# Performance work log

Hardware: AMD Instinct MI355X
Metric: run time of the kernel (lower is better)

## Reference

```python
import jax, jax.numpy as jnp
import numpy as np

B, T, IN_DIM = 32, 1024, 32
E, H, P = 256, 4, 32  # embed_dim, heads, max_patches
HD = E // H


def _lin(x, w, b):
    # torch nn.Linear: y = x @ W.T + b, W: [out, in]
    return jnp.einsum('...i,oi->...o', x, w) + b


def setup_inputs() -> dict:
    key = jax.random.key(0)
    ks = jax.random.split(key, 13)
    s = 0.02
    return {
        'x': jax.random.normal(ks[0], (B, T, IN_DIM), jnp.float32),
        'ip_w': jax.random.normal(ks[1], (E, IN_DIM), jnp.float32) * s,
        'ip_b': jnp.zeros((E,), jnp.float32),
        'in_proj_w': jax.random.normal(ks[2], (3 * E, E), jnp.float32) * s,
        'in_proj_b': jnp.zeros((3 * E,), jnp.float32),
        'out_w': jax.random.normal(ks[3], (E, E), jnp.float32) * s,
        'out_b': jnp.zeros((E,), jnp.float32),
        'bp_w1': jax.random.normal(ks[4], (32, E), jnp.float32) * s,
        'bp_b1': jnp.zeros((32,), jnp.float32),
        'bp_w2': jax.random.normal(ks[5], (1, 32), jnp.float32) * s,
        'bp_b2': jnp.zeros((1,), jnp.float32),
        'pr_w': jax.random.normal(ks[6], (E, E), jnp.float32) * s,
        'pr_b': jnp.zeros((E,), jnp.float32),
    }


def reference(x, ip_w, ip_b, in_proj_w, in_proj_b, out_w, out_b,
              bp_w1, bp_b1, bp_w2, bp_b2, pr_w, pr_b):
    # input projection
    h = _lin(x, ip_w, ip_b)  # [B,T,E]
    # MultiheadAttention (self-attn, batch_first, eval/no-dropout)
    qkv = _lin(h, in_proj_w, in_proj_b)  # [B,T,3E]
    q, k, v = jnp.split(qkv, 3, axis=-1)
    q = q.reshape(B, T, H, HD)
    k = k.reshape(B, T, H, HD)
    v = v.reshape(B, T, H, HD)
    scores = jnp.einsum('bqhd,bkhd->bhqk', q, k) / jnp.sqrt(jnp.float32(HD))
    attn = jax.nn.softmax(scores, axis=-1)
    ctx = jnp.einsum('bhqk,bkhd->bqhd', attn, v).reshape(B, T, E)
    attn_out = _lin(ctx, out_w, out_b)  # [B,T,E]
    # boundary scores
    bscore = jax.nn.sigmoid(_lin(jax.nn.relu(_lin(attn_out, bp_w1, bp_b1)), bp_w2, bp_b2))[..., 0]  # [B,T]
    cbp = jnp.cumsum(bscore, axis=1)
    cbp = cbp / (cbp[:, -1:] + 1e-6)
    pid = jnp.minimum(jnp.floor(cbp * P).astype(jnp.int32), P - 1)  # [B,T]
    # segment-mean pooling via scatter-add
    b_idx = jnp.broadcast_to(jnp.arange(B)[:, None], (B, T))
    pe = jnp.zeros((B, P, E), attn_out.dtype).at[b_idx, pid].add(attn_out)
    cnt = jnp.zeros((B, P), attn_out.dtype).at[b_idx, pid].add(1.0)
    pe = pe / jnp.clip(cnt, 1.0)[..., None]
    return _lin(pe, pr_w, pr_b)  # [B,P,E]
```

## Files before the change

### kernel.cpp

```cpp
#include <hip/hip_runtime.h>
#include <math.h>

constexpr int Bn  = 32;
constexpr int Tn  = 1024;
constexpr int INn = 32;
constexpr int En  = 256;
constexpr int Pn  = 32;

typedef short bf16x8 __attribute__((ext_vector_type(8)));
typedef float f32x4  __attribute__((ext_vector_type(4)));

__device__ __forceinline__ unsigned short f2bf(float f) {
    unsigned int b = __float_as_uint(f);
    b += 0x7FFF + ((b >> 16) & 1);
    return (unsigned short)(b >> 16);
}
__device__ __forceinline__ float bf2f(unsigned short h) {
    return __uint_as_float(((unsigned int)h) << 16);
}

__global__ __launch_bounds__(256) void k_prep(const float* __restrict__ ipw,
                                              const float* __restrict__ ipb,
                                              const float* __restrict__ inw,
                                              const float* __restrict__ inb,
                                              const float* __restrict__ outw,
                                              const float* __restrict__ w1,
                                              unsigned short* __restrict__ Wcb,
                                              float* __restrict__ bc,
                                              unsigned short* __restrict__ Wb,
                                              unsigned short* __restrict__ w1h,
                                              unsigned short* __restrict__ w1l) {
    int blk = blockIdx.x, tid = threadIdx.x;
    if (blk < 96) {
        int idx = blk * 256 + tid;
        int o = idx >> 5, i = idx & 31;
        const float* wr = inw + (size_t)o * En;
        float a0 = 0.f, a1 = 0.f;
        for (int e = 0; e < En; e += 2) {
            a0 += wr[e]     * ipw[(size_t)e * INn + i];
            a1 += wr[e + 1] * ipw[(size_t)(e + 1) * INn + i];
        }
        Wcb[(size_t)o * INn + i] = f2bf(a0 + a1);
    } else if (blk < 99) {
        int o = (blk - 96) * 256 + tid;
        const float* wr = inw + (size_t)o * En;
        float a = inb[o];
        for (int e = 0; e < En; ++e) a += wr[e] * ipb[e];
        bc[o] = a;
    } else if (blk < 163) {
        int idx = (blk - 99) * 256 + tid;
        float4 a = *(const float4*)(outw + (size_t)idx * 4);
        unsigned int u0 = f2bf(a.x) | ((unsigned int)f2bf(a.y) << 16);
        unsigned int u1 = f2bf(a.z) | ((unsigned int)f2bf(a.w) << 16);
        *(uint2*)(Wb + (size_t)idx * 4) = make_uint2(u0, u1);
    } else {
        int idx = (blk - 163) * 256 + tid;
        float a = w1[idx];
        unsigned short h = f2bf(a);
        w1h[idx] = h;
        w1l[idx] = f2bf(a - bf2f(h));
    }
}

__global__ __launch_bounds__(256, 2) void k_qkv(const float* __restrict__ x,
                                                const unsigned short* __restrict__ Wcb,
                                                const float* __restrict__ bc,
                                                unsigned short* __restrict__ Qb,
                                                unsigned short* __restrict__ Kb,
                                                unsigned short* __restrict__ Vt) {
    int tid = threadIdx.x;
    int wv = tid >> 6, lane = tid & 63;
    int cl = lane & 15, quad = lane >> 4;
    int m0 = blockIdx.x * 64;
    int b = m0 >> 10, tl0 = m0 & 1023;
    int n0w = wv * 192;
    f32x4 zero4 = {0.f, 0.f, 0.f, 0.f};

    bf16x8 wfrag[12]; float bv[12];
#pragma unroll
    for (int nt = 0; nt < 12; ++nt) {
        int col = n0w + nt * 16 + cl;
        wfrag[nt] = *(const bf16x8*)(Wcb + (size_t)col * 32 + quad * 8);
        bv[nt] = bc[col];
    }
#pragma unroll
    for (int mt = 0; mt < 4; ++mt) {
        const float* xr = x + (size_t)(m0 + mt * 16 + cl) * 32 + quad * 8;
        float4 xa = *(const float4*)xr, xc = *(const float4*)(xr + 4);
        bf16x8 af;
        af[0] = (short)f2bf(xa.x); af[1] = (short)f2bf(xa.y);
        af[2] = (short)f2bf(xa.z); af[3] = (short)f2bf(xa.w);
        af[4] = (short)f2bf(xc.x); af[5] = (short)f2bf(xc.y);
        af[6] = (short)f2bf(xc.z); af[7] = (short)f2bf(xc.w);
        f32x4 acc[12];
#pragma unroll
        for (int nt = 0; nt < 12; ++nt)
            acc[nt] = __builtin_amdgcn_mfma_f32_16x16x32_bf16(af, wfrag[nt], zero4, 0, 0, 0);
        int tloc = tl0 + mt * 16 + quad * 4;
#pragma unroll
        for (int nt = 0; nt < 12; ++nt) {
            int col = n0w + nt * 16 + cl;
            int slot = col >> 8, c = col & 255;
            int h = c >> 6, d = c & 63;
            int bh = b * 4 + h;
            if (slot == 2) {
                unsigned int u0 = f2bf(acc[nt][0] + bv[nt]) |
                                  ((unsigned int)f2bf(acc[nt][1] + bv[nt]) << 16);
                unsigned int u1 = f2bf(acc[nt][2] + bv[nt]) |
                                  ((unsigned int)f2bf(acc[nt][3] + bv[nt]) << 16);
                *(uint2*)(Vt + ((size_t)bh * 64 + d) * 1024 + tloc) = make_uint2(u0, u1);
            } else {
                unsigned short* dst = (slot ? Kb : Qb) +
                                      ((size_t)bh * 1024 + tloc) * 64 + d;
#pragma unroll
                for (int r = 0; r < 4; ++r)
                    dst[(size_t)r * 64] = f2bf(acc[nt][r] + bv[nt]);
            }
        }
    }
}

__global__ __launch_bounds__(256, 4) void k_attn(const unsigned short* __restrict__ Qb,
                                                 const unsigned short* __restrict__ Kb,
                                                 const unsigned short* __restrict__ Vt,
                                                 unsigned short* __restrict__ Po0,
                                                 unsigned short* __restrict__ Po1,
                                                 float* __restrict__ L0,
                                                 float* __restrict__ L1) {
    __shared__ unsigned short Ks[64][72];
    __shared__ unsigned short Vs[64][72];
    __shared__ __align__(16) unsigned short Pl[4][2][16][40];
    int blk = blockIdx.x;
    int bh = blk & 127;
    int r_ = blk >> 7;
    int qb = r_ & 7, half = r_ >> 3;
    int b = bh >> 2, h = bh & 3;
    int tid = threadIdx.x;
    int wv = tid >> 6, lane = tid & 63;
    int cl = lane & 15, quad = lane >> 4;
    int qbase = qb * 128 + wv * 32;

    f32x4 zero4 = {0.f, 0.f, 0.f, 0.f};
    bf16x8 qfrag[2][2];
#pragma unroll
    for (int tt = 0; tt < 2; ++tt)
#pragma unroll
        for (int ch = 0; ch < 2; ++ch)
            qfrag[tt][ch] = *(const bf16x8*)(Qb +
                ((size_t)bh * 1024 + qbase + tt * 16 + cl) * 64 + ch * 32 + quad * 8);
    f32x4 acc[2][4];
#pragma unroll
    for (int tt = 0; tt < 2; ++tt)
#pragma unroll
        for (int dt = 0; dt < 4; ++dt) acc[tt][dt] = zero4;
    float l[2] = {0.f, 0.f};

    const unsigned short* Kbase = Kb + (size_t)bh * 65536;
    const unsigned short* Vbase = Vt + (size_t)bh * 65536;

    for (int kt = 0; kt < 8; ++kt) {
        int ktt = half * 8 + kt;
#pragma unroll
        for (int r = 0; r < 2; ++r) {
            int idx = r * 256 + tid; int row = idx >> 3, c16 = idx & 7;
            *(uint4*)&Ks[row][c16 * 8] =
                *(const uint4*)(Kbase + (size_t)(ktt * 64 + row) * 64 + c16 * 8);
            *(uint4*)&Vs[row][c16 * 8] =
                *(const uint4*)(Vbase + (size_t)row * 1024 + ktt * 64 + c16 * 8);
        }
        __syncthreads();
#pragma unroll
        for (int c = 0; c < 2; ++c) {
            bf16x8 ka0 = *(const bf16x8*)&Ks[c * 32 + cl][quad * 8];
            bf16x8 ka1 = *(const bf16x8*)&Ks[c * 32 + cl][32 + quad * 8];
            bf16x8 kb0 = *(const bf16x8*)&Ks[c * 32 + 16 + cl][quad * 8];
            bf16x8 kb1 = *(const bf16x8*)&Ks[c * 32 + 16 + cl][32 + quad * 8];
            bf16x8 va[4];
#pragma unroll
            for (int dt = 0; dt < 4; ++dt)
                va[dt] = *(const bf16x8*)&Vs[dt * 16 + cl][c * 32 + quad * 8];
#pragma unroll
            for (int tt = 0; tt < 2; ++tt) {
                f32x4 s0 = __builtin_amdgcn_mfma_f32_16x16x32_bf16(ka0, qfrag[tt][0], zero4, 0, 0, 0);
                s0 = __builtin_amdgcn_mfma_f32_16x16x32_bf16(ka1, qfrag[tt][1], s0, 0, 0, 0);
                f32x4 s1 = __builtin_amdgcn_mfma_f32_16x16x32_bf16(kb0, qfrag[tt][0], zero4, 0, 0, 0);
                s1 = __builtin_amdgcn_mfma_f32_16x16x32_bf16(kb1, qfrag[tt][1], s1, 0, 0, 0);
                float p0 = __expf(0.125f * s0[0]), p1 = __expf(0.125f * s0[1]);
                float p2 = __expf(0.125f * s0[2]), p3 = __expf(0.125f * s0[3]);
                float p4 = __expf(0.125f * s1[0]), p5 = __expf(0.125f * s1[1]);
                float p6 = __expf(0.125f * s1[2]), p7 = __expf(0.125f * s1[3]);
                l[tt] += ((p0 + p1) + (p2 + p3)) + ((p4 + p5) + (p6 + p7));
                unsigned int w0 = f2bf(p0) | ((unsigned int)f2bf(p1) << 16);
                unsigned int w1 = f2bf(p2) | ((unsigned int)f2bf(p3) << 16);
                unsigned int w2 = f2bf(p4) | ((unsigned int)f2bf(p5) << 16);
                unsigned int w3 = f2bf(p6) | ((unsigned int)f2bf(p7) << 16);
                *(uint2*)&Pl[wv][tt][cl][quad * 4]      = make_uint2(w0, w1);
                *(uint2*)&Pl[wv][tt][cl][16 + quad * 4] = make_uint2(w2, w3);
            }
            asm volatile("s_waitcnt lgkmcnt(0)" ::: "memory");
#pragma unroll
            for (int tt = 0; tt < 2; ++tt) {
                bf16x8 pf = *(const bf16x8*)&Pl[wv][tt][cl][quad * 8];
#pragma unroll
                for (int dt = 0; dt < 4; ++dt)
                    acc[tt][dt] = __builtin_amdgcn_mfma_f32_16x16x32_bf16(pf, va[dt], acc[tt][dt], 0, 0, 0);
            }
        }
        __syncthreads();
    }
#pragma unroll
    for (int tt = 0; tt < 2; ++tt) {
        l[tt] += __shfl_xor(l[tt], 16);
        l[tt] += __shfl_xor(l[tt], 32);
    }
    unsigned short* Po = half ? Po1 : Po0;
    float* Lp = half ? L1 : L0;
#pragma unroll
    for (int tt = 0; tt < 2; ++tt) {
#pragma unroll
        for (int r = 0; r < 4; ++r) {
            size_t row = (size_t)(b * 1024 + qbase + tt * 16 + quad * 4 + r) * En;
#pragma unroll
            for (int dt = 0; dt < 4; ++dt)
                Po[row + h * 64 + dt * 16 + cl] = f2bf(acc[tt][dt][r]);
        }
    }
    if (quad == 0) {
#pragma unroll
        for (int tt = 0; tt < 2; ++tt)
            Lp[bh * 1024 + qbase + tt * 16 + cl] = l[tt];
    }
}

__global__ __launch_bounds__(256) void k_out(const unsigned short* __restrict__ Po0,
                                             const unsigned short* __restrict__ Po1,
                                             const float* __restrict__ L0,
                                             const float* __restrict__ L1,
                                             const unsigned short* __restrict__ Wb,
                                             const float* __restrict__ bias,
                                             float* __restrict__ AO) {
    __shared__ unsigned short As[64][32];
    __shared__ unsigned short Bs[256][32];
    int tid = threadIdx.x;
    int wv = tid >> 6, lane = tid & 63;
    int cl = lane & 15, quad = lane >> 4;
    size_t m0 = (size_t)blockIdx.x * 64;

    f32x4 acc[4][4];
#pragma unroll
    for (int mt = 0; mt < 4; ++mt)
#pragma unroll
        for (int nt = 0; nt < 4; ++nt) acc[mt][nt] = {0.f, 0.f, 0.f, 0.f};

    for (int kt = 0; kt < 8; ++kt) {
        if (kt) __syncthreads();
        {
            int row = tid >> 2, c4 = tid & 3;
            size_t g = (m0 + row) * En + kt * 32 + c4 * 8;
            uint4 u0 = *(const uint4*)(Po0 + g);
            uint4 u1 = *(const uint4*)(Po1 + g);
            int gt = (int)(m0 + row);
            int li = ((gt >> 10) * 4 + (kt >> 1)) * 1024 + (gt & 1023);
            float linv = 1.f / (L0[li] + L1[li]);
            unsigned int a0[4] = {u0.x, u0.y, u0.z, u0.w};
            unsigned int a1[4] = {u1.x, u1.y, u1.z, u1.w};
            unsigned int w[4];
#pragma unroll
            for (int j = 0; j < 4; ++j) {
                float lo = (bf2f((unsigned short)(a0[j] & 0xffff)) +
                            bf2f((unsigned short)(a1[j] & 0xffff))) * linv;
                float hi = (bf2f((unsigned short)(a0[j] >> 16)) +
                            bf2f((unsigned short)(a1[j] >> 16))) * linv;
                w[j] = f2bf(lo) | ((unsigned int)f2bf(hi) << 16);
            }
            *(uint4*)&As[row][c4 * 8] = make_uint4(w[0], w[1], w[2], w[3]);
        }
#pragma unroll
        for (int j = 0; j < 4; ++j) {
            int lin = j * 256 + tid; int n = lin >> 2, c = lin & 3;
            *(uint4*)&Bs[n][c * 8] =
                *(const uint4*)(Wb + (size_t)n * En + kt * 32 + c * 8);
        }
        __syncthreads();
        bf16x8 af[4], bfr[4];
#pragma unroll
        for (int mt = 0; mt < 4; ++mt)
            af[mt] = *(const bf16x8*)&As[mt * 16 + cl][quad * 8];
#pragma unroll
        for (int nt = 0; nt < 4; ++nt)
            bfr[nt] = *(const bf16x8*)&Bs[wv * 64 + nt * 16 + cl][quad * 8];
#pragma unroll
        for (int mt = 0; mt < 4; ++mt)
#pragma unroll
            for (int nt = 0; nt < 4; ++nt)
                acc[mt][nt] = __builtin_amdgcn_mfma_f32_16x16x32_bf16(af[mt], bfr[nt], acc[mt][nt], 0, 0, 0);
    }
    float bv[4];
#pragma unroll
    for (int nt = 0; nt < 4; ++nt) bv[nt] = bias[wv * 64 + nt * 16 + cl];
#pragma unroll
    for (int mt = 0; mt < 4; ++mt)
#pragma unroll
        for (int nt = 0; nt < 4; ++nt)
#pragma unroll
            for (int r = 0; r < 4; ++r)
                AO[(m0 + mt * 16 + quad * 4 + r) * En + wv * 64 + nt * 16 + cl] =
                    acc[mt][nt][r] + bv[nt];
}

__global__ __launch_bounds__(256) void k_bscore(const float* __restrict__ AO,
                                                const unsigned short* __restrict__ w1h,
                                                const unsigned short* __restrict__ w1l,
                                                const float* __restrict__ b1,
                                                const float* __restrict__ w2,
                                                const float* __restrict__ b2,
                                                float* __restrict__ bsc) {
    __shared__ unsigned short Ah[128][72];
    __shared__ unsigned short Al[128][72];
    int tid = threadIdx.x;
    int wv = tid >> 6, lane = tid & 63;
    int cl = lane & 15, quad = lane >> 4;
    int m0 = blockIdx.x * 128;

    f32x4 acc[2][2];
#pragma unroll
    for (int mt = 0; mt < 2; ++mt)
#pragma unroll
        for (int nt = 0; nt < 2; ++nt) acc[mt][nt] = {0.f, 0.f, 0.f, 0.f};

    for (int kt = 0; kt < 4; ++kt) {
        if (kt) __syncthreads();
#pragma unroll
        for (int j = 0; j < 8; ++j) {
            int lin = j * 256 + tid; int row = lin >> 4, c4 = lin & 15;
            float4 a = *(const float4*)(AO + (size_t)(m0 + row) * En + kt * 64 + c4 * 4);
            unsigned short h0 = f2bf(a.x), h1v = f2bf(a.y), h2 = f2bf(a.z), h3 = f2bf(a.w);
            unsigned short l0 = f2bf(a.x - bf2f(h0)), l1v = f2bf(a.y - bf2f(h1v));
            unsigned short l2 = f2bf(a.z - bf2f(h2)), l3 = f2bf(a.w - bf2f(h3));
            *(uint2*)&Ah[row][c4 * 4] =
                make_uint2(h0 | ((unsigned int)h1v << 16), h2 | ((unsigned int)h3 << 16));
            *(uint2*)&Al[row][c4 * 4] =
                make_uint2(l0 | ((unsigned int)l1v << 16), l2 | ((unsigned int)l3 << 16));
        }
        __syncthreads();
#pragma unroll
        for (int ks = 0; ks < 2; ++ks) {
            bf16x8 bh_[2], bl_[2];
#pragma unroll
            for (int nt = 0; nt < 2; ++nt) {
                size_t off = (size_t)(nt * 16 + cl) * En + kt * 64 + ks * 32 + quad * 8;
                bh_[nt] = *(const bf16x8*)(w1h + off);
                bl_[nt] = *(const bf16x8*)(w1l + off);
            }
#pragma unroll
            for (int mt = 0; mt < 2; ++mt) {
                int row = wv * 32 + mt * 16 + cl;
                bf16x8 ah = *(const bf16x8*)&Ah[row][ks * 32 + quad * 8];
                bf16x8 al = *(const bf16x8*)&Al[row][ks * 32 + quad * 8];
#pragma unroll
                for (int nt = 0; nt < 2; ++nt) {
                    acc[mt][nt] = __builtin_amdgcn_mfma_f32_16x16x32_bf16(ah, bh_[nt], acc[mt][nt], 0, 0, 0);
                    acc[mt][nt] = __builtin_amdgcn_mfma_f32_16x16x32_bf16(ah, bl_[nt], acc[mt][nt], 0, 0, 0);
                    acc[mt][nt] = __builtin_amdgcn_mfma_f32_16x16x32_bf16(al, bh_[nt], acc[mt][nt], 0, 0, 0);
                }
            }
        }
    }
    float b1v[2], w2v[2];
#pragma unroll
    for (int nt = 0; nt < 2; ++nt) {
        b1v[nt] = b1[nt * 16 + cl];
        w2v[nt] = w2[nt * 16 + cl];
    }
    float b2v = b2[0];
#pragma unroll
    for (int mt = 0; mt < 2; ++mt) {
        f32x4 z;
#pragma unroll
        for (int r = 0; r < 4; ++r)
            z[r] = fmaxf(acc[mt][0][r] + b1v[0], 0.f) * w2v[0] +
                   fmaxf(acc[mt][1][r] + b1v[1], 0.f) * w2v[1];
#pragma unroll
        for (int d = 1; d < 16; d <<= 1)
#pragma unroll
            for (int r = 0; r < 4; ++r) z[r] += __shfl_xor(z[r], d);
        if (cl == 0) {
#pragma unroll
            for (int r = 0; r < 4; ++r)
                bsc[m0 + wv * 32 + mt * 16 + quad * 4 + r] =
                    1.f / (1.f + __expf(-(z[r] + b2v)));
        }
    }
}

__global__ __launch_bounds__(1024) void k_scan(const float* __restrict__ bsc,
                                               int* __restrict__ segs) {
    __shared__ float wsum[16];
    __shared__ float s_pre[1024];
    __shared__ float s_tot;
    int b = blockIdx.x, t = threadIdx.x;
    float x = bsc[b * Tn + t];
#pragma unroll
    for (int d = 1; d < 64; d <<= 1) {
        float y = __shfl_up(x, d);
        if ((t & 63) >= d) x += y;
    }
    int w = t >> 6;
    if ((t & 63) == 63) wsum[w] = x;
    __syncthreads();
    if (t == 0) {
        float s = 0.f;
        for (int i = 0; i < 16; ++i) { float tmp = wsum[i]; wsum[i] = s; s += tmp; }
        s_tot = s;
    }
    __syncthreads();
    float pre = x + wsum[w];
    s_pre[t] = pre;
    __syncthreads();
    float denom = s_tot + 1e-6f;
    float qv = pre / denom * 32.0f;
    int pid = min((int)floorf(qv), 31);
    int pidprev = -1;
    if (t > 0) {
        float qp = s_pre[t - 1] / denom * 32.0f;
        pidprev = min((int)floorf(qp), 31);
    }
    for (int p = pidprev + 1; p <= pid; ++p) segs[b * 33 + p] = t;
    if (t == 1023)
        for (int p = pid + 1; p <= 32; ++p) segs[b * 33 + p] = Tn;
}

__global__ __launch_bounds__(256) void k_pool_proj(const float* __restrict__ ao,
                                                   const int* __restrict__ segs,
                                                   const float* __restrict__ prw,
                                                   const float* __restrict__ prb,
                                                   float* __restrict__ out) {
    __shared__ float pes[En];
    int b = blockIdx.y, p = blockIdx.x;
    int s = segs[b * 33 + p];
    int e = segs[b * 33 + p + 1];
    int tid = threadIdx.x;
    float sum = 0.f;
    for (int t = s; t < e; ++t)
        sum += ao[((size_t)b * Tn + t) * En + tid];
    pes[tid] = sum / fmaxf((float)(e - s), 1.f);
    __syncthreads();
    float a0 = prb[tid], a1 = 0.f;
#pragma unroll
    for (int k = 0; k < En; k += 4) {
        float4 wv = *(const float4*)(prw + (size_t)tid * En + k);
        float4 pv = *(const float4*)&pes[k];
        a0 += wv.x * pv.x; a1 += wv.y * pv.y;
        a0 += wv.z * pv.z; a1 += wv.w * pv.w;
    }
    out[((size_t)b * Pn + p) * En + tid] = a0 + a1;
}

extern "C" void kernel_launch(void* const* d_in, const int* in_sizes, int n_in,
                              void* d_out, int out_size, void* d_ws, size_t ws_size,
                              hipStream_t stream) {
    const float* x    = (const float*)d_in[0];
    const float* ipw  = (const float*)d_in[1];
    const float* ipb  = (const float*)d_in[2];
    const float* inw  = (const float*)d_in[3];
    const float* inb  = (const float*)d_in[4];
    const float* outw = (const float*)d_in[5];
    const float* outb = (const float*)d_in[6];
    const float* bw1  = (const float*)d_in[7];
    const float* bb1  = (const float*)d_in[8];
    const float* bw2  = (const float*)d_in[9];
    const float* bb2  = (const float*)d_in[10];
    const float* prw  = (const float*)d_in[11];
    const float* prb  = (const float*)d_in[12];

    char* base = (char*)d_ws;
    unsigned short* Qb  = (unsigned short*)base;
    unsigned short* Kb  = Qb + (size_t)8388608;
    float*          AO  = (float*)base;
    unsigned short* Vt  = (unsigned short*)(base + (size_t)33554432);
    unsigned short* Po0 = (unsigned short*)(base + (size_t)50331648);
    unsigned short* Po1 = (unsigned short*)(base + (size_t)67108864);
    unsigned short* Wcb = (unsigned short*)(base + (size_t)83886080);
    float*          bc  = (float*)(base + (size_t)83935232);
    unsigned short* Wb  = (unsigned short*)(base + (size_t)83938304);
    unsigned short* w1h = (unsigned short*)(base + (size_t)84069376);
    unsigned short* w1l = (unsigned short*)(base + (size_t)84085760);
    float*          L0  = (float*)(base + (size_t)84102144);
    float*          L1  = (float*)(base + (size_t)84626432);
    float*          bsc = (float*)(base + (size_t)85150720);
    int*           segs = (int*)(base + (size_t)85281792);

    k_prep<<<195, 256, 0, stream>>>(ipw, ipb, inw, inb, outw, bw1,
                                    Wcb, bc, Wb, w1h, w1l);
    k_qkv<<<512, 256, 0, stream>>>(x, Wcb, bc, Qb, Kb, Vt);
    k_attn<<<2048, 256, 0, stream>>>(Qb, Kb, Vt, Po0, Po1, L0, L1);
    k_out<<<512, 256, 0, stream>>>(Po0, Po1, L0, L1, Wb, outb, AO);
    k_bscore<<<256, 256, 0, stream>>>(AO, w1h, w1l, bb1, bw2, bb2, bsc);
    k_scan<<<32, 1024, 0, stream>>>(bsc, segs);
    k_pool_proj<<<dim3(32, 32), 256, 0, stream>>>(AO, segs, prw, prb,
                                                  (float*)d_out);
}
```

Before: 237.8 us.

## Split pool/projection into MFMA split-bf16 GEMM and use truncating perm pack in attention

The fused pool+projection kernel, where each thread did a scalar 256-length dot product per patch, is split into a pooling kernel that writes patch means to workspace and a final kernel. The final kernel runs the 1024x256x256 projection with bf16 MFMA, using hi/lo weight and activation splits (three products) to keep accuracy close to fp32. The projection weights are pre-split in the prep kernel. Separately, attention probabilities are packed to bf16 with a byte-permute truncation instead of round-to-nearest, and the row sum is taken from the truncated values so it stays consistent. This adds a kernel launch and a PE round trip through memory, and the final GEMM only launches 16 blocks.

```diff
diff --git a/kernel.cpp b/kernel.cpp
--- a/kernel.cpp
+++ b/kernel.cpp
@@ -17,6 +17,10 @@
 }
 __device__ __forceinline__ float bf2f(unsigned short h) {
     return __uint_as_float(((unsigned int)h) << 16);
+}
+__device__ __forceinline__ unsigned int permpack(float lo, float hi) {
+    return __builtin_amdgcn_perm(__float_as_uint(hi), __float_as_uint(lo),
+                                 0x07060302u);
 }
 
 __global__ __launch_bounds__(256) void k_prep(const float* __restrict__ ipw,
@@ -25,11 +29,14 @@
                                               const float* __restrict__ inb,
                                               const float* __restrict__ outw,
                                               const float* __restrict__ w1,
+                                              const float* __restrict__ prw,
                                               unsigned short* __restrict__ Wcb,
                                               float* __restrict__ bc,
                                               unsigned short* __restrict__ Wb,
                                               unsigned short* __restrict__ w1h,
-                                              unsigned short* __restrict__ w1l) {
+                                              unsigned short* __restrict__ w1l,
+                                              unsigned short* __restrict__ pwh,
+                                              unsigned short* __restrict__ pwl) {
     int blk = blockIdx.x, tid = threadIdx.x;
     if (blk < 96) {
         int idx = blk * 256 + tid;
@@ -53,12 +60,18 @@
         unsigned int u0 = f2bf(a.x) | ((unsigned int)f2bf(a.y) << 16);
         unsigned int u1 = f2bf(a.z) | ((unsigned int)f2bf(a.w) << 16);
         *(uint2*)(Wb + (size_t)idx * 4) = make_uint2(u0, u1);
-    } else {
+    } else if (blk < 195) {
         int idx = (blk - 163) * 256 + tid;
         float a = w1[idx];
         unsigned short h = f2bf(a);
         w1h[idx] = h;
         w1l[idx] = f2bf(a - bf2f(h));
+    } else {
+        int idx = (blk - 195) * 256 + tid;
+        float a = prw[idx];
+        unsigned short h = f2bf(a);
+        pwh[idx] = h;
+        pwl[idx] = f2bf(a - bf2f(h));
     }
 }
 
@@ -189,11 +202,14 @@
                 float p2 = __expf(0.125f * s0[2]), p3 = __expf(0.125f * s0[3]);
                 float p4 = __expf(0.125f * s1[0]), p5 = __expf(0.125f * s1[1]);
                 float p6 = __expf(0.125f * s1[2]), p7 = __expf(0.125f * s1[3]);
-                l[tt] += ((p0 + p1) + (p2 + p3)) + ((p4 + p5) + (p6 + p7));
-                unsigned int w0 = f2bf(p0) | ((unsigned int)f2bf(p1) << 16);
-                unsigned int w1 = f2bf(p2) | ((unsigned int)f2bf(p3) << 16);
-                unsigned int w2 = f2bf(p4) | ((unsigned int)f2bf(p5) << 16);
-                unsigned int w3 = f2bf(p6) | ((unsigned int)f2bf(p7) << 16);
+                unsigned int w0 = permpack(p0, p1);
+                unsigned int w1 = permpack(p2, p3);
+                unsigned int w2 = permpack(p4, p5);
+                unsigned int w3 = permpack(p6, p7);
+                l[tt] += ((__uint_as_float(w0 << 16) + __uint_as_float(w0 & 0xffff0000u)) +
+                          (__uint_as_float(w1 << 16) + __uint_as_float(w1 & 0xffff0000u))) +
+                         ((__uint_as_float(w2 << 16) + __uint_as_float(w2 & 0xffff0000u)) +
+                          (__uint_as_float(w3 << 16) + __uint_as_float(w3 & 0xffff0000u)));
                 *(uint2*)&Pl[wv][tt][cl][quad * 4]      = make_uint2(w0, w1);
                 *(uint2*)&Pl[wv][tt][cl][16 + quad * 4] = make_uint2(w2, w3);
             }
@@ -430,12 +446,9 @@
         for (int p = pid + 1; p <= 32; ++p) segs[b * 33 + p] = Tn;
 }
 
-__global__ __launch_bounds__(256) void k_pool_proj(const float* __restrict__ ao,
-                                                   const int* __restrict__ segs,
-                                                   const float* __restrict__ prw,
-                                                   const float* __restrict__ prb,
-                                                   float* __restrict__ out) {
-    __shared__ float pes[En];
+__global__ __launch_bounds__(256) void k_pool(const float* __restrict__ ao,
+                                              const int* __restrict__ segs,
+                                              float* __restrict__ PE) {
     int b = blockIdx.y, p = blockIdx.x;
     int s = segs[b * 33 + p];
     int e = segs[b * 33 + p + 1];
@@ -443,17 +456,79 @@
     float sum = 0.f;
     for (int t = s; t < e; ++t)
         sum += ao[((size_t)b * Tn + t) * En + tid];
-    pes[tid] = sum / fmaxf((float)(e - s), 1.f);
-    __syncthreads();
-    float a0 = prb[tid], a1 = 0.f;
-#pragma unroll
-    for (int k = 0; k < En; k += 4) {
-        float4 wv = *(const float4*)(prw + (size_t)tid * En + k);
-        float4 pv = *(const float4*)&pes[k];
-        a0 += wv.x * pv.x; a1 += wv.y * pv.y;
-        a0 += wv.z * pv.z; a1 += wv.w * pv.w;
-    }
-    out[((size_t)b * Pn + p) * En + tid] = a0 + a1;
+    PE[(size_t)(b * Pn + p) * En + tid] = sum / fmaxf((float)(e - s), 1.f);
+}
+
+__global__ __launch_bounds__(256) void k_final(const float* __restrict__ PE,
+                                               const unsigned short* __restrict__ pwh,
+                                               const unsigned short* __restrict__ pwl,
+                                               const float* __restrict__ prb,
+                                               float* __restrict__ out) {
+    __shared__ unsigned short Ah[64][40];
+    __shared__ unsigned short Al[64][40];
+    int tid = threadIdx.x;
+    int wv = tid >> 6, lane = tid & 63;
+    int cl = lane & 15, quad = lane >> 4;
+    int m0 = blockIdx.x * 64;
+
+    f32x4 acc[4][4];
+#pragma unroll
+    for (int mt = 0; mt < 4; ++mt)
+#pragma unroll
+        for (int nt = 0; nt < 4; ++nt) acc[mt][nt] = {0.f, 0.f, 0.f, 0.f};
+
+    for (int kt = 0; kt < 8; ++kt) {
+        if (kt) __syncthreads();
+        {
+            int row = tid >> 2, c8 = (tid & 3) * 8;
+            const float* src = PE + (size_t)(m0 + row) * En + kt * 32 + c8;
+            float4 a = *(const float4*)src, b4 = *(const float4*)(src + 4);
+            float v[8] = {a.x, a.y, a.z, a.w, b4.x, b4.y, b4.z, b4.w};
+            unsigned int hw[4], lw[4];
+#pragma unroll
+            for (int j = 0; j < 4; ++j) {
+                unsigned short h0 = f2bf(v[2 * j]), h1 = f2bf(v[2 * j + 1]);
+                unsigned short q0 = f2bf(v[2 * j] - bf2f(h0));
+                unsigned short q1 = f2bf(v[2 * j + 1] - bf2f(h1));
+                hw[j] = h0 | ((unsigned int)h1 << 16);
+                lw[j] = q0 | ((unsigned int)q1 << 16);
+            }
+            *(uint4*)&Ah[row][c8] = make_uint4(hw[0], hw[1], hw[2], hw[3]);
+            *(uint4*)&Al[row][c8] = make_uint4(lw[0], lw[1], lw[2], lw[3]);
+        }
+        __syncthreads();
+        bf16x8 ah[4], al[4], bh_[4], bl_[4];
+#pragma unroll
+        for (int mt = 0; mt < 4; ++mt) {
+            ah[mt] = *(const bf16x8*)&Ah[mt * 16 + cl][quad * 8];
+            al[mt] = *(const bf16x8*)&Al[mt * 16 + cl][quad * 8];
+        }
+#pragma unroll
+        for (int nt = 0; nt < 4; ++nt) {
+            size_t off = (size_t)(wv * 64 + nt * 16 + cl) * En + kt * 32 + quad * 8;
+            bh_[nt] = *(const bf16x8*)(pwh + off);
+            bl_[nt] = *(const bf16x8*)(pwl + off);
+        }
+#pragma unroll
+        for (int mt = 0; mt < 4; ++mt)
+#pragma unroll
+            for (int nt = 0; nt < 4; ++nt) {
+                acc[mt][nt] = __builtin_amdgcn_mfma_f32_16x16x32_bf16(ah[mt], bh_[nt], acc[mt][nt], 0, 0, 0);
+                acc[mt][nt] = __builtin_amdgcn_mfma_f32_16x16x32_bf16(ah[mt], bl_[nt], acc[mt][nt], 0, 0, 0);
+                acc[mt][nt] = __builtin_amdgcn_mfma_f32_16x16x32_bf16(al[mt], bh_[nt], acc[mt][nt], 0, 0, 0);
+            }
+    }
+    float bv[4];
+#pragma unroll
+    for (int nt = 0; nt < 4; ++nt) bv[nt] = prb[wv * 64 + nt * 16 + cl];
+#pragma unroll
+    for (int mt = 0; mt < 4; ++mt)
+#pragma unroll
+        for (int nt = 0; nt < 4; ++nt)
+#pragma unroll
+            for (int r = 0; r < 4; ++r)
+                out[(size_t)(m0 + mt * 16 + quad * 4 + r) * En + wv * 64 + nt * 16 + cl] =
+                    acc[mt][nt][r] + bv[nt];
 }
 
 extern "C" void kernel_launch(void* const* d_in, const int* in_sizes, int n_in,
@@ -478,6 +553,7 @@
     unsigned short* Kb  = Qb + (size_t)8388608;
     float*          AO  = (float*)base;
     unsigned short* Vt  = (unsigned short*)(base + (size_t)33554432);
+    float*          PE  = (float*)(base + (size_t)33554432);
     unsigned short* Po0 = (unsigned short*)(base + (size_t)50331648);
     unsigned short* Po1 = (unsigned short*)(base + (size_t)67108864);
     unsigned short* Wcb = (unsigned short*)(base + (size_t)83886080);
@@ -489,14 +565,16 @@
     float*          L1  = (float*)(base + (size_t)84626432);
     float*          bsc = (float*)(base + (size_t)85150720);
     int*           segs = (int*)(base + (size_t)85281792);
-
-    k_prep<<<195, 256, 0, stream>>>(ipw, ipb, inw, inb, outw, bw1,
-                                    Wcb, bc, Wb, w1h, w1l);
+    unsigned short* pwh = (unsigned short*)(base + (size_t)85286912);
+    unsigned short* pwl = (unsigned short*)(base + (size_t)85417984);
+
+    k_prep<<<451, 256, 0, stream>>>(ipw, ipb, inw, inb, outw, bw1, prw,
+                                    Wcb, bc, Wb, w1h, w1l, pwh, pwl);
     k_qkv<<<512, 256, 0, stream>>>(x, Wcb, bc, Qb, Kb, Vt);
     k_attn<<<2048, 256, 0, stream>>>(Qb, Kb, Vt, Po0, Po1, L0, L1);
     k_out<<<512, 256, 0, stream>>>(Po0, Po1, L0, L1, Wb, outb, AO);
     k_bscore<<<256, 256, 0, stream>>>(AO, w1h, w1l, bb1, bw2, bb2, bsc);
     k_scan<<<32, 1024, 0, stream>>>(bsc, segs);
-    k_pool_proj<<<dim3(32, 32), 256, 0, stream>>>(AO, segs, prw, prb,
-                                                  (float*)d_out);
-}
+    k_pool<<<dim3(32, 32), 256, 0, stream>>>(AO, segs, PE);
+    k_final<<<16, 256, 0, stream>>>(PE, pwh, pwl, prb, (float*)d_out);
+}
```

Result: faster. 218.0 us (-8.3%).
